# Optimization experiments

Measured on AMD Instinct MI355X. Metric: run time of the kernel, lower is better.

Reference implementation:

```python
import jax, jax.numpy as jnp
import numpy as np

NUM_SEQS = 4      # number of prefill sequences (equal-length ragged batch)
SEQ_LEN = 4096    # tokens per sequence
HIDDEN = 2048     # config.hidden_size
CONV_DIM = 2048   # config.conv_dim
K = 4             # config.conv_kernel_size


def setup_inputs() -> dict:
    key = jax.random.key(0)
    k1, k2, k3, k4 = jax.random.split(key, 4)
    hidden_states = jax.random.normal(k1, (NUM_SEQS * SEQ_LEN, HIDDEN), jnp.float32)
    w_in = jax.random.normal(k2, (3 * CONV_DIM, HIDDEN), jnp.float32) * 0.02
    conv_weight = jax.random.normal(k3, (CONV_DIM, 1, K), jnp.float32) * 0.5
    w_out = jax.random.normal(k4, (HIDDEN, CONV_DIM), jnp.float32) * 0.02
    return {"hidden_states": hidden_states, "w_in": w_in,
            "conv_weight": conv_weight, "w_out": w_out}


def reference(hidden_states, w_in, conv_weight, w_out):
    # in_proj: [N, H] @ [H, 3D] -> [N, 3D]; chunk into b, c, x
    bcx = hidden_states @ w_in.T
    b, c, x = jnp.split(bcx, 3, axis=-1)
    bx = b * x  # gated input, [N, D]

    # Prefill causal depthwise conv per sequence (no prior state -> zero left pad).
    # Pack to [S, D, L] and run one grouped conv for all sequences at once
    # (equivalent to the per-sequence F.conv1d loop with padding=K-1, truncated to L).
    bx_sdl = bx.reshape(NUM_SEQS, SEQ_LEN, CONV_DIM).transpose(0, 2, 1)  # [S, D, L]
    conv_out = jax.lax.conv_general_dilated(
        bx_sdl, conv_weight,
        window_strides=(1,), padding=[(K - 1, 0)],
        dimension_numbers=("NCH", "OIH", "NCH"),
        feature_group_count=CONV_DIM,
    )  # [S, D, L]
    conv_out = conv_out.transpose(0, 2, 1).reshape(-1, CONV_DIM)  # [N, D]

    y = c * conv_out                 # BCx gating
    out = y @ w_out.T                # out_proj -> [N, H]

    # Final conv state per sequence: last K-1 gated inputs (seq_len >= K-1 branch).
    new_states = bx.reshape(NUM_SEQS, SEQ_LEN, CONV_DIM)[:, -(K - 1):, :]  # [S, K-1, D]
    return out, new_states
```

## Files before the change

kernel.cpp:

```cpp
#include <hip/hip_runtime.h>
#include <stdint.h>

#define NUM_SEQS 4
#define SEQ_LEN  4096
#define HIDDEN   2048
#define CONV_DIM 2048
#define NTOK     (NUM_SEQS * SEQ_LEN)
#define N3D      (3 * CONV_DIM)

typedef unsigned short u16;
typedef unsigned int   u32;
typedef __bf16 bf16x8 __attribute__((ext_vector_type(8)));
typedef float  f32x16 __attribute__((ext_vector_type(16)));

__device__ __forceinline__ u16 f2bf(float f) {
  union { float f; u32 u; } v; v.f = f;
  u32 u = v.u;
  u += 0x7fffu + ((u >> 16) & 1u);
  return (u16)(u >> 16);
}

__device__ __forceinline__ void async16(const void* g, void* l) {
  __builtin_amdgcn_global_load_lds(
      (const __attribute__((address_space(1))) u32*)g,
      (__attribute__((address_space(3))) u32*)l, 16, 0, 0);
}

__global__ __launch_bounds__(256) void cast_f32_bf16(
    const float* __restrict__ in, u16* __restrict__ out, int n4)
{
  int i = blockIdx.x * 256 + threadIdx.x;
  if (i >= n4) return;
  float4 f = ((const float4*)in)[i];
  ushort4 o;
  o.x = f2bf(f.x); o.y = f2bf(f.y); o.z = f2bf(f.z); o.w = f2bf(f.w);
  ((ushort4*)out)[i] = o;
}

template<bool OUT_BF16>
__global__ __launch_bounds__(512, 2) void gemm256_bt(
    const u16* __restrict__ A, const u16* __restrict__ B, void* __restrict__ Cv,
    const int M, const int N, const int K)
{
  __shared__ u16 sm[65536];
  u16* ldsA = &sm[0];
  u16* ldsB = &sm[32768];

  const int tid  = threadIdx.x;
  const int lane = tid & 63;
  const int wave = tid >> 6;
  const int l32  = lane & 31;
  const int hl   = lane >> 5;
  const int wm   = wave >> 2;
  const int wn   = wave & 3;
  (void)M;

  const int gx  = gridDim.x;
  const int nwg = gx * gridDim.y;
  const int orig = blockIdx.y * gx + blockIdx.x;
  const int cpx  = nwg >> 3;
  const int swz  = (orig & 7) * cpx + (orig >> 3);
  const int nBase = (swz % gx) * 256;
  const int mBase = (swz / gx) * 256;

  const int NT = K >> 6;

  const int rowS = ((tid >> 8) & 1) * 32 + (tid & 31);
  const int gsel = ((tid >> 6) & 3) * 2 + ((tid >> 5) & 1);
  const u16* aTB = A + (size_t)(mBase + rowS) * K + gsel * 8;
  const u16* bTB = B + (size_t)(nBase + rowS) * K + gsel * 8;
  const size_t C1 = (size_t)64 * K;

#define STAGE(ldsO, gBase, tl, h) do {                                        \
    const int _b = (tl) & 1;                                                  \
    u16* _d = (ldsO) + _b * 16384 + (h) * 8192 + tid * 8;                     \
    const u16* _s = (gBase) + (size_t)(h) * 128 * K + (size_t)(tl) * 64;      \
    async16(_s, _d);                                                          \
    async16(_s + C1, _d + 4096);                                              \
  } while (0)

  const int aG = wm * 4;
  const int bG = wn * 2;
  const int lo = lane * 8;

#define LDA(mt, ks, b) (*(const bf16x8*)&ldsA[(b) * 16384 + (aG + (mt)) * 2048 + (ks) * 512 + lo])
#define LDB(nt, ks, b) (*(const bf16x8*)&ldsB[(b) * 16384 + (bG + (nt)) * 2048 + (ks) * 512 + lo])

  f32x16 acc[4][2];
#pragma unroll
  for (int i = 0; i < 4; ++i)
#pragma unroll
    for (int j = 0; j < 2; ++j)
#pragma unroll
      for (int r = 0; r < 16; ++r) acc[i][j][r] = 0.f;

  STAGE(ldsA, aTB, 0, 0); STAGE(ldsA, aTB, 0, 1);
  STAGE(ldsB, bTB, 0, 0); STAGE(ldsB, bTB, 0, 1);
  STAGE(ldsB, bTB, 1, 0); STAGE(ldsB, bTB, 1, 1);
  asm volatile("s_waitcnt vmcnt(4)" ::: "memory");
  __builtin_amdgcn_s_barrier();
  __builtin_amdgcn_sched_barrier(0);

  bf16x8 aF[2][4], bF[2][4];

#pragma unroll 2
  for (int t = 0; t < NT; ++t) {
    const int buf = t & 1;

    if (t + 1 < NT) STAGE(ldsA, aTB, t + 1, 0);
#pragma unroll
    for (int ks = 0; ks < 4; ++ks) {
      aF[0][ks] = LDA(0, ks, buf);
      aF[1][ks] = LDA(1, ks, buf);
      bF[0][ks] = LDB(0, ks, buf);
    }
#pragma unroll
    for (int ks = 0; ks < 4; ++ks) bF[1][ks] = LDB(1, ks, buf);
    __builtin_amdgcn_sched_barrier(0);
    __builtin_amdgcn_s_barrier();
    __builtin_amdgcn_sched_barrier(0);
    __builtin_amdgcn_s_setprio(1);
#pragma unroll
    for (int ks = 0; ks < 4; ++ks) {
      acc[0][0] = __builtin_amdgcn_mfma_f32_32x32x16_bf16(aF[0][ks], bF[0][ks], acc[0][0], 0, 0, 0);
      acc[1][0] = __builtin_amdgcn_mfma_f32_32x32x16_bf16(aF[1][ks], bF[0][ks], acc[1][0], 0, 0, 0);
    }
    __builtin_amdgcn_s_setprio(0);
    __builtin_amdgcn_sched_barrier(0);
    __builtin_amdgcn_s_barrier();
    __builtin_amdgcn_sched_barrier(0);

    if (t + 1 < NT) STAGE(ldsA, aTB, t + 1, 1);
    __builtin_amdgcn_sched_barrier(0);
    __builtin_amdgcn_s_barrier();
    __builtin_amdgcn_sched_barrier(0);
    __builtin_amdgcn_s_setprio(1);
#pragma unroll
    for (int ks = 0; ks < 4; ++ks) {
      acc[0][1] = __builtin_amdgcn_mfma_f32_32x32x16_bf16(aF[0][ks], bF[1][ks], acc[0][1], 0, 0, 0);
      acc[1][1] = __builtin_amdgcn_mfma_f32_32x32x16_bf16(aF[1][ks], bF[1][ks], acc[1][1], 0, 0, 0);
    }
    __builtin_amdgcn_s_setprio(0);
    __builtin_amdgcn_sched_barrier(0);
    __builtin_amdgcn_s_barrier();
    __builtin_amdgcn_sched_barrier(0);

    if (t + 2 < NT) STAGE(ldsB, bTB, t + 2, 0);
#pragma unroll
    for (int ks = 0; ks < 4; ++ks) {
      aF[0][ks] = LDA(2, ks, buf);
      aF[1][ks] = LDA(3, ks, buf);
    }
    __builtin_amdgcn_sched_barrier(0);
    __builtin_amdgcn_s_barrier();
    __builtin_amdgcn_sched_barrier(0);
    __builtin_amdgcn_s_setprio(1);
#pragma unroll
    for (int ks = 0; ks < 4; ++ks) {
      acc[2][1] = __builtin_amdgcn_mfma_f32_32x32x16_bf16(aF[0][ks], bF[1][ks], acc[2][1], 0, 0, 0);
      acc[3][1] = __builtin_amdgcn_mfma_f32_32x32x16_bf16(aF[1][ks], bF[1][ks], acc[3][1], 0, 0, 0);
    }
    __builtin_amdgcn_s_setprio(0);
    __builtin_amdgcn_sched_barrier(0);
    __builtin_amdgcn_s_barrier();
    __builtin_amdgcn_sched_barrier(0);

    if (t + 2 < NT) STAGE(ldsB, bTB, t + 2, 1);
    if (t < NT - 2) asm volatile("s_waitcnt vmcnt(4)" ::: "memory");
    else            asm volatile("s_waitcnt vmcnt(0)" ::: "memory");
    __builtin_amdgcn_sched_barrier(0);
    __builtin_amdgcn_s_barrier();
    __builtin_amdgcn_sched_barrier(0);
    __builtin_amdgcn_s_setprio(1);
#pragma unroll
    for (int ks = 0; ks < 4; ++ks) {
      acc[2][0] = __builtin_amdgcn_mfma_f32_32x32x16_bf16(aF[0][ks], bF[0][ks], acc[2][0], 0, 0, 0);
      acc[3][0] = __builtin_amdgcn_mfma_f32_32x32x16_bf16(aF[1][ks], bF[0][ks], acc[3][0], 0, 0, 0);
    }
    __builtin_amdgcn_s_setprio(0);
    __builtin_amdgcn_sched_barrier(0);
    __builtin_amdgcn_s_barrier();
    __builtin_amdgcn_sched_barrier(0);
  }
#undef STAGE
#undef LDA
#undef LDB

#pragma unroll
  for (int mt = 0; mt < 4; ++mt) {
#pragma unroll
    for (int nt = 0; nt < 2; ++nt) {
      const int col = nBase + wn * 64 + nt * 32 + l32;
#pragma unroll
      for (int r = 0; r < 16; ++r) {
        const int row = mBase + wm * 128 + mt * 32 + (r & 3) + 8 * (r >> 2) + 4 * hl;
        if (OUT_BF16)
          ((u16*)Cv)[(size_t)row * N + col] = f2bf(acc[mt][nt][r]);
        else
          ((float*)Cv)[(size_t)row * N + col] = acc[mt][nt][r];
      }
    }
  }
}

#define TT 32
__global__ __launch_bounds__(256) void conv_gate(
    const u16* __restrict__ bcx, const float* __restrict__ convw,
    u16* __restrict__ y, float* __restrict__ states)
{
  const int tid = threadIdx.x;
  const int d8  = tid * 8;
  const int s   = blockIdx.y;
  const int t0  = blockIdx.x * TT;

  float w0[8], w1[8], w2[8], w3[8];
#pragma unroll
  for (int j = 0; j < 8; ++j) {
    float4 wv = *(const float4*)&convw[(d8 + j) * 4];
    w0[j] = wv.x; w1[j] = wv.y; w2[j] = wv.z; w3[j] = wv.w;
  }

  float win0[8], win1[8], win2[8];
  if (t0 == 0) {
#pragma unroll
    for (int j = 0; j < 8; ++j) { win0[j] = 0.f; win1[j] = 0.f; win2[j] = 0.f; }
  } else {
    const u16* r0 = bcx + (size_t)(s * SEQ_LEN + t0 - 3) * N3D + d8;
    bf16x8 b0 = *(const bf16x8*)(r0);
    bf16x8 x0 = *(const bf16x8*)(r0 + 2 * CONV_DIM);
    bf16x8 b1 = *(const bf16x8*)(r0 + N3D);
    bf16x8 x1 = *(const bf16x8*)(r0 + N3D + 2 * CONV_DIM);
    bf16x8 b2 = *(const bf16x8*)(r0 + 2 * N3D);
    bf16x8 x2 = *(const bf16x8*)(r0 + 2 * N3D + 2 * CONV_DIM);
#pragma unroll
    for (int j = 0; j < 8; ++j) {
      win0[j] = (float)b0[j] * (float)x0[j];
      win1[j] = (float)b1[j] * (float)x1[j];
      win2[j] = (float)b2[j] * (float)x2[j];
    }
  }

  for (int t = t0; t < t0 + TT; ++t) {
    const u16* row = bcx + (size_t)(s * SEQ_LEN + t) * N3D + d8;
    bf16x8 bv = *(const bf16x8*)row;
    bf16x8 cv = *(const bf16x8*)(row + CONV_DIM);
    bf16x8 xv = *(const bf16x8*)(row + 2 * CONV_DIM);
    float bx[8];
#pragma unroll
    for (int j = 0; j < 8; ++j) bx[j] = (float)bv[j] * (float)xv[j];

    u32 pk[4];
#pragma unroll
    for (int j = 0; j < 4; ++j) {
      const int a = 2 * j, b = 2 * j + 1;
      float ya = (float)cv[a] * (w0[a]*win0[a] + w1[a]*win1[a] + w2[a]*win2[a] + w3[a]*bx[a]);
      float yb = (float)cv[b] * (w0[b]*win0[b] + w1[b]*win1[b] + w2[b]*win2[b] + w3[b]*bx[b]);
      pk[j] = (u32)f2bf(ya) | ((u32)f2bf(yb) << 16);
    }
    uint4 o; o.x = pk[0]; o.y = pk[1]; o.z = pk[2]; o.w = pk[3];
    *(uint4*)&y[(size_t)(s * SEQ_LEN + t) * CONV_DIM + d8] = o;

    if (t >= SEQ_LEN - 3) {
      float* st = states + (size_t)(s * 3 + (t - (SEQ_LEN - 3))) * CONV_DIM + d8;
      float4 s0v; s0v.x = bx[0]; s0v.y = bx[1]; s0v.z = bx[2]; s0v.w = bx[3];
      float4 s1v; s1v.x = bx[4]; s1v.y = bx[5]; s1v.z = bx[6]; s1v.w = bx[7];
      *(float4*)st = s0v;
      *(float4*)(st + 4) = s1v;
    }
#pragma unroll
    for (int j = 0; j < 8; ++j) { win0[j] = win1[j]; win1[j] = win2[j]; win2[j] = bx[j]; }
  }
}

extern "C" void kernel_launch(void* const* d_in, const int* in_sizes, int n_in,
                              void* d_out, int out_size, void* d_ws, size_t ws_size,
                              hipStream_t stream)
{
  const float* hidden = (const float*)d_in[0];
  const float* w_in   = (const float*)d_in[1];
  const float* convw  = (const float*)d_in[2];
  const float* w_out  = (const float*)d_in[3];

  char* ws = (char*)d_ws;
  u16* hb  = (u16*)(ws);
  u16* wib = (u16*)(ws + (size_t)67108864);
  u16* wob = (u16*)(ws + (size_t)92274688);
  u16* bcx = (u16*)(ws + (size_t)100663296);
  u16* yb  = (u16*)(ws + (size_t)301989888);

  float* out    = (float*)d_out;
  float* states = out + (size_t)NTOK * HIDDEN;

  cast_f32_bf16<<<32768, 256, 0, stream>>>(hidden, hb, 8388608);
  cast_f32_bf16<<<12288, 256, 0, stream>>>(w_in,  wib, 3145728);
  cast_f32_bf16<<<4096,  256, 0, stream>>>(w_out, wob, 1048576);

  gemm256_bt<true><<<dim3(N3D / 256, NTOK / 256), 512, 0, stream>>>(
      hb, wib, bcx, NTOK, N3D, HIDDEN);

  conv_gate<<<dim3(SEQ_LEN / TT, NUM_SEQS), 256, 0, stream>>>(bcx, convw, yb, states);

  gemm256_bt<false><<<dim3(CONV_DIM / 256, NTOK / 256), 512, 0, stream>>>(
      yb, wob, out, NTOK, CONV_DIM, CONV_DIM);
}
```

Baseline: 912.1 us.

## Halve GEMM K-tile, triple-buffer B and prefetch fragments across phases

Reworks the 256x256 bf16 GEMM main loop to use 32-wide K tiles instead of 64, cutting LDS from 128KB to 80KB. A is double-buffered and B is triple-buffered with rotating pointers. The next tile's A/B fragments are loaded during the current MFMA phases to hide LDS latency. The smaller footprint may allow higher occupancy, at the cost of twice as many loop iterations and barriers per K.

```diff
diff --git a/kernel.cpp b/kernel.cpp
--- a/kernel.cpp
+++ b/kernel.cpp
@@ -42,9 +42,9 @@
     const u16* __restrict__ A, const u16* __restrict__ B, void* __restrict__ Cv,
     const int M, const int N, const int K)
 {
-  __shared__ u16 sm[65536];
+  __shared__ u16 sm[40960];
   u16* ldsA = &sm[0];
-  u16* ldsB = &sm[32768];
+  u16* ldsB = &sm[16384];
 
   const int tid  = threadIdx.x;
   const int lane = tid & 63;
@@ -63,28 +63,29 @@
   const int nBase = (swz % gx) * 256;
   const int mBase = (swz / gx) * 256;
 
-  const int NT = K >> 6;
-
-  const int rowS = ((tid >> 8) & 1) * 32 + (tid & 31);
-  const int gsel = ((tid >> 6) & 3) * 2 + ((tid >> 5) & 1);
-  const u16* aTB = A + (size_t)(mBase + rowS) * K + gsel * 8;
-  const u16* bTB = B + (size_t)(nBase + rowS) * K + gsel * 8;
-  const size_t C1 = (size_t)64 * K;
-
-#define STAGE(ldsO, gBase, tl, h) do {                                        \
-    const int _b = (tl) & 1;                                                  \
-    u16* _d = (ldsO) + _b * 16384 + (h) * 8192 + tid * 8;                     \
-    const u16* _s = (gBase) + (size_t)(h) * 128 * K + (size_t)(tl) * 64;      \
-    async16(_s, _d);                                                          \
-    async16(_s + C1, _d + 4096);                                              \
+  const int NT = K >> 5;
+
+  const int rowS = ((tid >> 7) & 3) * 32 + (tid & 31);
+  const int kcol = ((tid >> 6) & 1) * 16 + ((tid >> 5) & 1) * 8;
+  const u16* aTB = A + (size_t)(mBase + rowS) * K + kcol;
+  const u16* bTB = B + (size_t)(nBase + rowS) * K + kcol;
+  const size_t C1 = (size_t)128 * K;
+
+#define STAGE_A(bsel, tl) do {                                   \
+    u16* _d = ldsA + (bsel) * 8192 + tid * 8;                    \
+    const u16* _s = aTB + (size_t)(tl) * 32;                     \
+    async16(_s, _d); async16(_s + C1, _d + 4096);                \
   } while (0)
-
-  const int aG = wm * 4;
-  const int bG = wn * 2;
+#define STAGE_B(bptr, tl) do {                                   \
+    u16* _d = (bptr) + tid * 8;                                  \
+    const u16* _s = bTB + (size_t)(tl) * 32;                     \
+    async16(_s, _d); async16(_s + C1, _d + 4096);                \
+  } while (0)
+
   const int lo = lane * 8;
-
-#define LDA(mt, ks, b) (*(const bf16x8*)&ldsA[(b) * 16384 + (aG + (mt)) * 2048 + (ks) * 512 + lo])
-#define LDB(nt, ks, b) (*(const bf16x8*)&ldsB[(b) * 16384 + (bG + (nt)) * 2048 + (ks) * 512 + lo])
+#define LDA(g, ks, bsel) (*(const bf16x8*)&ldsA[(bsel) * 8192 + ((g) * 2 + (ks)) * 512 + lo])
+#define LDB(g, ks, bptr) (*(const bf16x8*)&(bptr)[((g) * 2 + (ks)) * 512 + lo])
+#define MFMA(a, b, c) __builtin_amdgcn_mfma_f32_32x32x16_bf16((a), (b), (c), 0, 0, 0)
 
   f32x16 acc[4][2];
 #pragma unroll
@@ -94,97 +95,105 @@
 #pragma unroll
       for (int r = 0; r < 16; ++r) acc[i][j][r] = 0.f;
 
-  STAGE(ldsA, aTB, 0, 0); STAGE(ldsA, aTB, 0, 1);
-  STAGE(ldsB, bTB, 0, 0); STAGE(ldsB, bTB, 0, 1);
-  STAGE(ldsB, bTB, 1, 0); STAGE(ldsB, bTB, 1, 1);
-  asm volatile("s_waitcnt vmcnt(4)" ::: "memory");
+  u16* bC  = ldsB;
+  u16* bN  = ldsB + 8192;
+  u16* bNN = ldsB + 16384;
+
+  STAGE_A(0, 0);
+  STAGE_B(bC, 0);
+  STAGE_B(bN, 1);
+  asm volatile("s_waitcnt vmcnt(2)" ::: "memory");
   __builtin_amdgcn_s_barrier();
   __builtin_amdgcn_sched_barrier(0);
 
-  bf16x8 aF[2][4], bF[2][4];
-
-#pragma unroll 2
-  for (int t = 0; t < NT; ++t) {
-    const int buf = t & 1;
-
-    if (t + 1 < NT) STAGE(ldsA, aTB, t + 1, 0);
-#pragma unroll
-    for (int ks = 0; ks < 4; ++ks) {
-      aF[0][ks] = LDA(0, ks, buf);
-      aF[1][ks] = LDA(1, ks, buf);
-      bF[0][ks] = LDB(0, ks, buf);
-    }
-#pragma unroll
-    for (int ks = 0; ks < 4; ++ks) bF[1][ks] = LDB(1, ks, buf);
-    __builtin_amdgcn_sched_barrier(0);
-    __builtin_amdgcn_s_barrier();
-    __builtin_amdgcn_sched_barrier(0);
-    __builtin_amdgcn_s_setprio(1);
-#pragma unroll
-    for (int ks = 0; ks < 4; ++ks) {
-      acc[0][0] = __builtin_amdgcn_mfma_f32_32x32x16_bf16(aF[0][ks], bF[0][ks], acc[0][0], 0, 0, 0);
-      acc[1][0] = __builtin_amdgcn_mfma_f32_32x32x16_bf16(aF[1][ks], bF[0][ks], acc[1][0], 0, 0, 0);
-    }
-    __builtin_amdgcn_s_setprio(0);
-    __builtin_amdgcn_sched_barrier(0);
-    __builtin_amdgcn_s_barrier();
-    __builtin_amdgcn_sched_barrier(0);
-
-    if (t + 1 < NT) STAGE(ldsA, aTB, t + 1, 1);
-    __builtin_amdgcn_sched_barrier(0);
-    __builtin_amdgcn_s_barrier();
-    __builtin_amdgcn_sched_barrier(0);
-    __builtin_amdgcn_s_setprio(1);
-#pragma unroll
-    for (int ks = 0; ks < 4; ++ks) {
-      acc[0][1] = __builtin_amdgcn_mfma_f32_32x32x16_bf16(aF[0][ks], bF[1][ks], acc[0][1], 0, 0, 0);
-      acc[1][1] = __builtin_amdgcn_mfma_f32_32x32x16_bf16(aF[1][ks], bF[1][ks], acc[1][1], 0, 0, 0);
-    }
-    __builtin_amdgcn_s_setprio(0);
-    __builtin_amdgcn_sched_barrier(0);
-    __builtin_amdgcn_s_barrier();
-    __builtin_amdgcn_sched_barrier(0);
-
-    if (t + 2 < NT) STAGE(ldsB, bTB, t + 2, 0);
-#pragma unroll
-    for (int ks = 0; ks < 4; ++ks) {
-      aF[0][ks] = LDA(2, ks, buf);
-      aF[1][ks] = LDA(3, ks, buf);
-    }
-    __builtin_amdgcn_sched_barrier(0);
-    __builtin_amdgcn_s_barrier();
-    __builtin_amdgcn_sched_barrier(0);
-    __builtin_amdgcn_s_setprio(1);
-#pragma unroll
-    for (int ks = 0; ks < 4; ++ks) {
-      acc[2][1] = __builtin_amdgcn_mfma_f32_32x32x16_bf16(aF[0][ks], bF[1][ks], acc[2][1], 0, 0, 0);
-      acc[3][1] = __builtin_amdgcn_mfma_f32_32x32x16_bf16(aF[1][ks], bF[1][ks], acc[3][1], 0, 0, 0);
-    }
-    __builtin_amdgcn_s_setprio(0);
-    __builtin_amdgcn_sched_barrier(0);
-    __builtin_amdgcn_s_barrier();
-    __builtin_amdgcn_sched_barrier(0);
-
-    if (t + 2 < NT) STAGE(ldsB, bTB, t + 2, 1);
-    if (t < NT - 2) asm volatile("s_waitcnt vmcnt(4)" ::: "memory");
-    else            asm volatile("s_waitcnt vmcnt(0)" ::: "memory");
-    __builtin_amdgcn_sched_barrier(0);
-    __builtin_amdgcn_s_barrier();
-    __builtin_amdgcn_sched_barrier(0);
-    __builtin_amdgcn_s_setprio(1);
-#pragma unroll
-    for (int ks = 0; ks < 4; ++ks) {
-      acc[2][0] = __builtin_amdgcn_mfma_f32_32x32x16_bf16(aF[0][ks], bF[0][ks], acc[2][0], 0, 0, 0);
-      acc[3][0] = __builtin_amdgcn_mfma_f32_32x32x16_bf16(aF[1][ks], bF[0][ks], acc[3][0], 0, 0, 0);
-    }
-    __builtin_amdgcn_s_setprio(0);
-    __builtin_amdgcn_sched_barrier(0);
-    __builtin_amdgcn_s_barrier();
-    __builtin_amdgcn_sched_barrier(0);
-  }
-#undef STAGE
+  bf16x8 a01F[2][2], a23F[2][2], b0F[2][2], b1F[2];
+#pragma unroll
+  for (int mt = 0; mt < 2; ++mt)
+#pragma unroll
+    for (int ks = 0; ks < 2; ++ks)
+      a01F[mt][ks] = LDA(wm * 4 + mt, ks, 0);
+#pragma unroll
+  for (int ks = 0; ks < 2; ++ks) b0F[0][ks] = LDB(wn * 2, ks, bC);
+
+  for (int t2 = 0; t2 < NT; t2 += 2) {
+#pragma unroll
+    for (int u = 0; u < 2; ++u) {
+      const int t = t2 + u;
+
+      if (t + 1 < NT) STAGE_A(u ^ 1, t + 1);
+#pragma unroll
+      for (int ks = 0; ks < 2; ++ks) b1F[ks] = LDB(wn * 2 + 1, ks, bC);
+#pragma unroll
+      for (int mt = 0; mt < 2; ++mt)
+#pragma unroll
+        for (int ks = 0; ks < 2; ++ks) a23F[mt][ks] = LDA(wm * 4 + 2 + mt, ks, u);
+      __builtin_amdgcn_sched_barrier(0);
+      __builtin_amdgcn_s_barrier();
+      __builtin_amdgcn_sched_barrier(0);
+      __builtin_amdgcn_s_setprio(1);
+#pragma unroll
+      for (int ks = 0; ks < 2; ++ks) {
+        acc[0][0] = MFMA(a01F[0][ks], b0F[u][ks], acc[0][0]);
+        acc[1][0] = MFMA(a01F[1][ks], b0F[u][ks], acc[1][0]);
+      }
+      __builtin_amdgcn_s_setprio(0);
+
+      __builtin_amdgcn_sched_barrier(0);
+      __builtin_amdgcn_s_barrier();
+      __builtin_amdgcn_sched_barrier(0);
+      __builtin_amdgcn_s_setprio(1);
+#pragma unroll
+      for (int ks = 0; ks < 2; ++ks) {
+        acc[0][1] = MFMA(a01F[0][ks], b1F[ks], acc[0][1]);
+        acc[1][1] = MFMA(a01F[1][ks], b1F[ks], acc[1][1]);
+      }
+      __builtin_amdgcn_s_setprio(0);
+
+      if (t + 2 < NT) {
+        STAGE_B(bNN, t + 2);
+        asm volatile("s_waitcnt vmcnt(2)" ::: "memory");
+      } else {
+        asm volatile("s_waitcnt vmcnt(0)" ::: "memory");
+      }
+      __builtin_amdgcn_sched_barrier(0);
+      __builtin_amdgcn_s_barrier();
+      __builtin_amdgcn_sched_barrier(0);
+      if (t + 1 < NT) {
+#pragma unroll
+        for (int mt = 0; mt < 2; ++mt)
+#pragma unroll
+          for (int ks = 0; ks < 2; ++ks)
+            a01F[mt][ks] = LDA(wm * 4 + mt, ks, u ^ 1);
+#pragma unroll
+        for (int ks = 0; ks < 2; ++ks) b0F[u ^ 1][ks] = LDB(wn * 2, ks, bN);
+      }
+      __builtin_amdgcn_s_setprio(1);
+#pragma unroll
+      for (int ks = 0; ks < 2; ++ks) {
+        acc[2][1] = MFMA(a23F[0][ks], b1F[ks], acc[2][1]);
+        acc[3][1] = MFMA(a23F[1][ks], b1F[ks], acc[3][1]);
+      }
+      __builtin_amdgcn_s_setprio(0);
+
+      __builtin_amdgcn_sched_barrier(0);
+      __builtin_amdgcn_s_barrier();
+      __builtin_amdgcn_sched_barrier(0);
+      __builtin_amdgcn_s_setprio(1);
+#pragma unroll
+      for (int ks = 0; ks < 2; ++ks) {
+        acc[2][0] = MFMA(a23F[0][ks], b0F[u][ks], acc[2][0]);
+        acc[3][0] = MFMA(a23F[1][ks], b0F[u][ks], acc[3][0]);
+      }
+      __builtin_amdgcn_s_setprio(0);
+
+      u16* _tmp = bC; bC = bN; bN = bNN; bNN = _tmp;
+    }
+  }
+#undef STAGE_A
+#undef STAGE_B
 #undef LDA
 #undef LDB
+#undef MFMA
 
 #pragma unroll
   for (int mt = 0; mt < 4; ++mt) {
```

New measurement: 960.2 us. 1.05x slower.

## Simplify GEMM main loop to one-tile-ahead prefetch with two barriers per tile

Applied to the files above, without the earlier changes.

Replaces the hand-tuned 8-phase ping-pong schedule (sched_barriers, setprio, staggered A/B staging with B two tiles ahead) with a simpler loop. It stages the whole next tile, waits for the current one, and then lets the compiler schedule the LDS reads and MFMAs freely. This is meant to cut barrier and scheduling-fence overhead and give the compiler room to interleave. The trade-off is that memory latency is hidden by only one tile of lookahead and the explicit MFMA/load interleaving is lost. Buffer indexing now relies on NT being even.

```diff
diff --git a/kernel.cpp b/kernel.cpp
--- a/kernel.cpp
+++ b/kernel.cpp
@@ -75,16 +75,19 @@
     const int _b = (tl) & 1;                                                  \
     u16* _d = (ldsO) + _b * 16384 + (h) * 8192 + tid * 8;                     \
     const u16* _s = (gBase) + (size_t)(h) * 128 * K + (size_t)(tl) * 64;      \
-    async16(_s, _d);                                                          \
-    async16(_s + C1, _d + 4096);                                              \
+    async16(_s, _d); async16(_s + C1, _d + 4096);                             \
+  } while (0)
+#define STAGE_TILE(tl) do {                                                   \
+    STAGE(ldsA, aTB, tl, 0); STAGE(ldsA, aTB, tl, 1);                         \
+    STAGE(ldsB, bTB, tl, 0); STAGE(ldsB, bTB, tl, 1);                         \
   } while (0)
 
   const int aG = wm * 4;
   const int bG = wn * 2;
   const int lo = lane * 8;
-
-#define LDA(mt, ks, b) (*(const bf16x8*)&ldsA[(b) * 16384 + (aG + (mt)) * 2048 + (ks) * 512 + lo])
-#define LDB(nt, ks, b) (*(const bf16x8*)&ldsB[(b) * 16384 + (bG + (nt)) * 2048 + (ks) * 512 + lo])
+#define LDA(g, ks, b) (*(const bf16x8*)&ldsA[(b) * 16384 + (g) * 2048 + (ks) * 512 + lo])
+#define LDB(g, ks, b) (*(const bf16x8*)&ldsB[(b) * 16384 + (g) * 2048 + (ks) * 512 + lo])
+#define MFMA(a, b, c) __builtin_amdgcn_mfma_f32_32x32x16_bf16((a), (b), (c), 0, 0, 0)
 
   f32x16 acc[4][2];
 #pragma unroll
@@ -94,97 +97,66 @@
 #pragma unroll
       for (int r = 0; r < 16; ++r) acc[i][j][r] = 0.f;
 
-  STAGE(ldsA, aTB, 0, 0); STAGE(ldsA, aTB, 0, 1);
-  STAGE(ldsB, bTB, 0, 0); STAGE(ldsB, bTB, 0, 1);
-  STAGE(ldsB, bTB, 1, 0); STAGE(ldsB, bTB, 1, 1);
-  asm volatile("s_waitcnt vmcnt(4)" ::: "memory");
-  __builtin_amdgcn_s_barrier();
-  __builtin_amdgcn_sched_barrier(0);
-
-  bf16x8 aF[2][4], bF[2][4];
-
-#pragma unroll 2
-  for (int t = 0; t < NT; ++t) {
-    const int buf = t & 1;
-
-    if (t + 1 < NT) STAGE(ldsA, aTB, t + 1, 0);
-#pragma unroll
-    for (int ks = 0; ks < 4; ++ks) {
-      aF[0][ks] = LDA(0, ks, buf);
-      aF[1][ks] = LDA(1, ks, buf);
-      bF[0][ks] = LDB(0, ks, buf);
-    }
-#pragma unroll
-    for (int ks = 0; ks < 4; ++ks) bF[1][ks] = LDB(1, ks, buf);
-    __builtin_amdgcn_sched_barrier(0);
-    __builtin_amdgcn_s_barrier();
-    __builtin_amdgcn_sched_barrier(0);
-    __builtin_amdgcn_s_setprio(1);
-#pragma unroll
-    for (int ks = 0; ks < 4; ++ks) {
-      acc[0][0] = __builtin_amdgcn_mfma_f32_32x32x16_bf16(aF[0][ks], bF[0][ks], acc[0][0], 0, 0, 0);
-      acc[1][0] = __builtin_amdgcn_mfma_f32_32x32x16_bf16(aF[1][ks], bF[0][ks], acc[1][0], 0, 0, 0);
-    }
-    __builtin_amdgcn_s_setprio(0);
-    __builtin_amdgcn_sched_barrier(0);
-    __builtin_amdgcn_s_barrier();
-    __builtin_amdgcn_sched_barrier(0);
-
-    if (t + 1 < NT) STAGE(ldsA, aTB, t + 1, 1);
-    __builtin_amdgcn_sched_barrier(0);
-    __builtin_amdgcn_s_barrier();
-    __builtin_amdgcn_sched_barrier(0);
-    __builtin_amdgcn_s_setprio(1);
-#pragma unroll
-    for (int ks = 0; ks < 4; ++ks) {
-      acc[0][1] = __builtin_amdgcn_mfma_f32_32x32x16_bf16(aF[0][ks], bF[1][ks], acc[0][1], 0, 0, 0);
-      acc[1][1] = __builtin_amdgcn_mfma_f32_32x32x16_bf16(aF[1][ks], bF[1][ks], acc[1][1], 0, 0, 0);
-    }
-    __builtin_amdgcn_s_setprio(0);
-    __builtin_amdgcn_sched_barrier(0);
-    __builtin_amdgcn_s_barrier();
-    __builtin_amdgcn_sched_barrier(0);
-
-    if (t + 2 < NT) STAGE(ldsB, bTB, t + 2, 0);
-#pragma unroll
-    for (int ks = 0; ks < 4; ++ks) {
-      aF[0][ks] = LDA(2, ks, buf);
-      aF[1][ks] = LDA(3, ks, buf);
-    }
-    __builtin_amdgcn_sched_barrier(0);
-    __builtin_amdgcn_s_barrier();
-    __builtin_amdgcn_sched_barrier(0);
-    __builtin_amdgcn_s_setprio(1);
-#pragma unroll
-    for (int ks = 0; ks < 4; ++ks) {
-      acc[2][1] = __builtin_amdgcn_mfma_f32_32x32x16_bf16(aF[0][ks], bF[1][ks], acc[2][1], 0, 0, 0);
-      acc[3][1] = __builtin_amdgcn_mfma_f32_32x32x16_bf16(aF[1][ks], bF[1][ks], acc[3][1], 0, 0, 0);
-    }
-    __builtin_amdgcn_s_setprio(0);
-    __builtin_amdgcn_sched_barrier(0);
-    __builtin_amdgcn_s_barrier();
-    __builtin_amdgcn_sched_barrier(0);
-
-    if (t + 2 < NT) STAGE(ldsB, bTB, t + 2, 1);
-    if (t < NT - 2) asm volatile("s_waitcnt vmcnt(4)" ::: "memory");
-    else            asm volatile("s_waitcnt vmcnt(0)" ::: "memory");
-    __builtin_amdgcn_sched_barrier(0);
-    __builtin_amdgcn_s_barrier();
-    __builtin_amdgcn_sched_barrier(0);
-    __builtin_amdgcn_s_setprio(1);
-#pragma unroll
-    for (int ks = 0; ks < 4; ++ks) {
-      acc[2][0] = __builtin_amdgcn_mfma_f32_32x32x16_bf16(aF[0][ks], bF[0][ks], acc[2][0], 0, 0, 0);
-      acc[3][0] = __builtin_amdgcn_mfma_f32_32x32x16_bf16(aF[1][ks], bF[0][ks], acc[3][0], 0, 0, 0);
-    }
-    __builtin_amdgcn_s_setprio(0);
-    __builtin_amdgcn_sched_barrier(0);
-    __builtin_amdgcn_s_barrier();
-    __builtin_amdgcn_sched_barrier(0);
+  STAGE_TILE(0);
+
+  for (int t2 = 0; t2 < NT; t2 += 2) {
+#pragma unroll
+    for (int u = 0; u < 2; ++u) {
+      const int t = t2 + u;
+
+      if (t + 1 < NT) {
+        STAGE_TILE(t + 1);
+        asm volatile("s_waitcnt vmcnt(8)" ::: "memory");
+      } else {
+        asm volatile("s_waitcnt vmcnt(0)" ::: "memory");
+      }
+      __builtin_amdgcn_s_barrier();
+
+      bf16x8 aF[2][4], bF0[4], bF1[4];
+#pragma unroll
+      for (int ks = 0; ks < 4; ++ks) {
+        aF[0][ks] = LDA(aG + 0, ks, u);
+        aF[1][ks] = LDA(aG + 1, ks, u);
+        bF0[ks]   = LDB(bG + 0, ks, u);
+      }
+#pragma unroll
+      for (int ks = 0; ks < 4; ++ks) bF1[ks] = LDB(bG + 1, ks, u);
+
+#pragma unroll
+      for (int ks = 0; ks < 4; ++ks) {
+        acc[0][0] = MFMA(aF[0][ks], bF0[ks], acc[0][0]);
+        acc[1][0] = MFMA(aF[1][ks], bF0[ks], acc[1][0]);
+      }
+#pragma unroll
+      for (int ks = 0; ks < 4; ++ks) {
+        acc[0][1] = MFMA(aF[0][ks], bF1[ks], acc[0][1]);
+        acc[1][1] = MFMA(aF[1][ks], bF1[ks], acc[1][1]);
+      }
+
+#pragma unroll
+      for (int ks = 0; ks < 4; ++ks) {
+        aF[0][ks] = LDA(aG + 2, ks, u);
+        aF[1][ks] = LDA(aG + 3, ks, u);
+      }
+#pragma unroll
+      for (int ks = 0; ks < 4; ++ks) {
+        acc[2][1] = MFMA(aF[0][ks], bF1[ks], acc[2][1]);
+        acc[3][1] = MFMA(aF[1][ks], bF1[ks], acc[3][1]);
+      }
+#pragma unroll
+      for (int ks = 0; ks < 4; ++ks) {
+        acc[2][0] = MFMA(aF[0][ks], bF0[ks], acc[2][0]);
+        acc[3][0] = MFMA(aF[1][ks], bF0[ks], acc[3][0]);
+      }
+
+      __builtin_amdgcn_s_barrier();
+    }
   }
 #undef STAGE
+#undef STAGE_TILE
 #undef LDA
 #undef LDB
+#undef MFMA
 
 #pragma unroll
   for (int mt = 0; mt < 4; ++mt) {
```

Result: slower. 933.1 us (+2.3%).
